# Performance work log

Measured on AMD Instinct MI355X. Metric: run time of the kernel, lower is better.

Reference implementation:

```python
import jax, jax.numpy as jnp
import numpy as np

N0, N1, N2 = 100000, 20000, 4000   # nodes per hierarchy level
F, H, C = 128, 128, 10             # num_features, hidden_dim, num_classes
E0, E1, E2 = 1600000, 320000, 64000  # intra-level edges (avg degree 16)
EPS = 1e-5                          # BatchNorm eps


def setup_inputs() -> dict:
    key = jax.random.key(0)
    ks = jax.random.split(key, 16)
    s = 0.05
    return {
        "x": jax.random.normal(ks[0], (N0, F), jnp.float32),
        "ei0": jax.random.randint(ks[1], (2, E0), 0, N0),
        "ei1": jax.random.randint(ks[2], (2, E1), 0, N1),
        "ei2": jax.random.randint(ks[3], (2, E2), 0, N2),
        "parent1": jax.random.randint(ks[4], (N0,), 0, N1),
        "parent2": jax.random.randint(ks[5], (N1,), 0, N2),
        "W0": jax.random.normal(ks[6], (F, H), jnp.float32) * s,
        "b0": jnp.zeros((H,), jnp.float32),
        "W1": jax.random.normal(ks[7], (H, H), jnp.float32) * s,
        "b1": jnp.zeros((H,), jnp.float32),
        "W2": jax.random.normal(ks[8], (H, H), jnp.float32) * s,
        "b2": jnp.zeros((H,), jnp.float32),
        "W3": jax.random.normal(ks[9], (2 * H, H), jnp.float32) * s,
        "b3": jnp.zeros((H,), jnp.float32),
        "W4": jax.random.normal(ks[10], (2 * H, C), jnp.float32) * s,
        "b4": jnp.zeros((C,), jnp.float32),
        "pW": jax.random.normal(ks[11], (4, H, H), jnp.float32) * s,
        "pb": jnp.zeros((4, H), jnp.float32),
        "pgamma": jnp.ones((4, H), jnp.float32),
        "pbeta": jnp.zeros((4, H), jnp.float32),
        "pmean": jax.random.normal(ks[12], (4, H), jnp.float32) * 0.1,
        "pvar": jax.random.uniform(ks[13], (4, H), jnp.float32, 0.5, 1.5),
    }


def _gcn(x, ei, W, b):
    # GCNConv: add self loops, symmetric D^-1/2 (A+I) D^-1/2 normalization.
    n = x.shape[0]
    loops = jnp.arange(n)
    row = jnp.concatenate([ei[0], loops])  # source nodes
    col = jnp.concatenate([ei[1], loops])  # target nodes
    deg = jax.ops.segment_sum(jnp.ones(row.shape, x.dtype), col, num_segments=n)
    dis = deg ** -0.5  # deg >= 1 because of self loops
    norm = dis[row] * dis[col]
    xw = x @ W
    out = jax.ops.segment_sum(norm[:, None] * xw[row], col, num_segments=n)
    return out + b


def _pool_nn(y, W, b, g, beta, mean, var):
    # SEPooling nn: Linear -> ReLU -> BatchNorm1d (eval mode, running stats)
    y = jax.nn.relu(y @ W + b)
    return (y - mean) * (g / jnp.sqrt(var + EPS)) + beta


def reference(x, ei0, ei1, ei2, parent1, parent2,
              W0, b0, W1, b1, W2, b2, W3, b3, W4, b4,
              pW, pb, pgamma, pbeta, pmean, pvar):
    relu = jax.nn.relu
    # down path (dropout is identity in eval mode)
    h0 = relu(_gcn(x, ei0, W0, b0))  # [N0,H]; stored skip xs[0]
    p = jax.ops.segment_sum(h0, parent1, num_segments=N1)  # scatter-add children -> parents
    x1 = relu(_pool_nn(p, pW[0], pb[0], pgamma[0], pbeta[0], pmean[0], pvar[0]))
    h1 = relu(_gcn(x1, ei1, W1, b1))  # [N1,H]; stored skip xs[1]
    p = jax.ops.segment_sum(h1, parent2, num_segments=N2)
    x2 = relu(_pool_nn(p, pW[1], pb[1], pgamma[1], pbeta[1], pmean[1], pvar[1]))
    # up path: conv, unpool (gather parent feature per child), concat skip
    h = relu(_gcn(x2, ei2, W2, b2))  # [N2,H]
    xu = relu(_pool_nn(h[parent2], pW[2], pb[2], pgamma[2], pbeta[2], pmean[2], pvar[2]))  # [N1,H]
    xc = jnp.concatenate([xu, h1], axis=1)  # [N1,2H]
    h = relu(_gcn(xc, ei1, W3, b3))  # [N1,H]
    xu = relu(_pool_nn(h[parent1], pW[3], pb[3], pgamma[3], pbeta[3], pmean[3], pvar[3]))  # [N0,H]
    xc = jnp.concatenate([xu, h0], axis=1)  # [N0,2H]
    out = _gcn(xc, ei0, W4, b4)  # [N0,C]
    return jax.nn.log_softmax(out, axis=-1)
```

## Files before the change

### kernel.cpp

```cpp
#include <hip/hip_runtime.h>
#include <math.h>

#define N0 100000
#define N1 20000
#define N2 4000
#define HDIM 128
#define E0C 1600000
#define E1C 320000
#define E2C 64000
#define EPSBN 1e-5f

typedef unsigned int u32;
typedef float f32x4 __attribute__((ext_vector_type(4)));
typedef short bf16x8 __attribute__((ext_vector_type(8)));

union FragU { uint4 u; bf16x8 h; };
__device__ __forceinline__ bf16x8 asbf(uint4 v) { FragU x; x.u = v; return x.h; }

__device__ __forceinline__ float bl(u32 p) { return __uint_as_float(p << 16); }
__device__ __forceinline__ float bh(u32 p) { return __uint_as_float(p & 0xFFFF0000u); }
__device__ __forceinline__ u32 pack2(float a, float b) {
    u32 ua = __float_as_uint(a), ub = __float_as_uint(b);
    ua = (ua + 0x7FFFu + ((ua >> 16) & 1u)) >> 16;
    ub = (ub + 0x7FFFu + ((ub >> 16) & 1u)) >> 16;
    return ua | (ub << 16);
}

#define OFF0 0
#define OFF1 (N0)
#define OFF2 (N0 + N1)
#define OFF3 (N0 + N1 + N2)
#define OFF4 (N0 + N1 + N2 + N1)
#define OFFT (N0 + N1 + N2 + N1 + N2)

#define S0 (E0C)
#define S1 (E0C + E1C)
#define S2 (E0C + E1C + E2C)
#define S3 (E0C + E1C + E2C + N0)
#define S4 (E0C + E1C + E2C + N0 + N1)

#define NBUCK ((OFFT + 1023) / 1024)
#define ITEMS_PER_BLK 2048
#define NBA ((S4 + ITEMS_PER_BLK - 1) / ITEMS_PER_BLK)
#define BH_N (NBUCK * NBA)
#define NBLK2 ((BH_N + 1023) / 1024)

#define NWMAT 9


__device__ __forceinline__ void item_full(int g,
    const int* __restrict__ ei0r, const int* __restrict__ ei0c,
    const int* __restrict__ ei1r, const int* __restrict__ ei1c,
    const int* __restrict__ ei2r, const int* __restrict__ ei2c,
    const int* __restrict__ p1, const int* __restrict__ p2,
    int& concat, int& payload)
{
    if (g < S0)      { concat = ei0c[g];             payload = ei0r[g]; }
    else if (g < S1) { int i = g - S0; concat = OFF1 + ei1c[i]; payload = ei1r[i]; }
    else if (g < S2) { int i = g - S1; concat = OFF2 + ei2c[i]; payload = ei2r[i]; }
    else if (g < S3) { int i = g - S2; concat = OFF3 + p1[i];   payload = i; }
    else             { int i = g - S3; concat = OFF4 + p2[i];   payload = i; }
}

__device__ __forceinline__ int item_concat(int g,
    const int* __restrict__ ei0c, const int* __restrict__ ei1c, const int* __restrict__ ei2c,
    const int* __restrict__ p1, const int* __restrict__ p2)
{
    if (g < S0)      return ei0c[g];
    else if (g < S1) return OFF1 + ei1c[g - S0];
    else if (g < S2) return OFF2 + ei2c[g - S1];
    else if (g < S3) return OFF3 + p1[g - S2];
    else             return OFF4 + p2[g - S3];
}

__global__ __launch_bounds__(256) void binhist_kernel(
    const int* __restrict__ ei0c, const int* __restrict__ ei1c, const int* __restrict__ ei2c,
    const int* __restrict__ p1, const int* __restrict__ p2,
    int* __restrict__ blockHist,
    const float* __restrict__ W0p, const float* __restrict__ W1p,
    const float* __restrict__ W2p, const float* __restrict__ W3p,
    const float* __restrict__ pWp, u32* __restrict__ Wpk)
{
    __shared__ int hist[NBUCK];
    int tid = threadIdx.x, blk = blockIdx.x;
    if (blk >= NBA) {
        int b = blk - NBA;
        const float* src;
        if (b == 0) src = W0p;
        else if (b == 1) src = W1p;
        else if (b == 2) src = W2p;
        else if (b == 3) src = W3p;
        else if (b == 4) src = W3p + 128 * 128;
        else src = pWp + (b - 5) * 128 * 128;
        u32* dst = Wpk + b * 8192;
        #pragma unroll
        for (int it = 0; it < 32; it++) {
            int flat = it * 256 + tid;
            int i = flat & 3;
            int ln = (flat >> 2) & 63;
            int s = (flat >> 8) & 3;
            int t = flat >> 10;
            int mm = ln & 15, qq = ln >> 4;
            int k0 = s * 32 + qq * 8 + 2 * i;
            int col = t * 16 + mm;
            dst[flat] = pack2(src[k0 * 128 + col], src[(k0 + 1) * 128 + col]);
        }
        return;
    }
    for (int i = tid; i < NBUCK; i += 256) hist[i] = 0;
    __syncthreads();
    int base = blk * ITEMS_PER_BLK;
    #pragma unroll
    for (int k = 0; k < ITEMS_PER_BLK / 256; k++) {
        int g = base + k * 256 + tid;
        if (g < S4) {
            int c = item_concat(g, ei0c, ei1c, ei2c, p1, p2);
            atomicAdd(&hist[c >> 10], 1);
        }
    }
    __syncthreads();
    for (int b = tid; b < NBUCK; b += 256) blockHist[b * NBA + blk] = hist[b];
}

__global__ __launch_bounds__(256) void scan_k1(const int* __restrict__ c, int* __restrict__ bsum, int n) {
    int t = threadIdx.x;
    int base = blockIdx.x * 1024 + t * 4;
    int s = 0;
    #pragma unroll
    for (int j = 0; j < 4; j++) {
        int idx = base + j;
        if (idx < n) s += c[idx];
    }
    #pragma unroll
    for (int o = 32; o > 0; o >>= 1) s += __shfl_down(s, o, 64);
    __shared__ int ws[4];
    if ((t & 63) == 0) ws[t >> 6] = s;
    __syncthreads();
    if (t == 0) bsum[blockIdx.x] = ws[0] + ws[1] + ws[2] + ws[3];
}

__global__ __launch_bounds__(256) void scan_k2(int* __restrict__ bsum, int* __restrict__ totalOut, int nb,
    const float* __restrict__ g, const float* __restrict__ beta,
    const float* __restrict__ mean, const float* __restrict__ var,
    float* __restrict__ scale, float* __restrict__ shift)
{
    int t = threadIdx.x;
    #pragma unroll
    for (int j = 0; j < 2; j++) {
        int i = j * 256 + t;
        float s = g[i] * rsqrtf(var[i] + EPSBN);
        scale[i] = s;
        shift[i] = beta[i] - mean[i] * s;
    }
    int v = (t < nb) ? bsum[t] : 0;
    __shared__ int ts[256];
    ts[t] = v;
    __syncthreads();
    for (int o = 1; o < 256; o <<= 1) {
        int u = (t >= o) ? ts[t - o] : 0;
        __syncthreads();
        ts[t] += u;
        __syncthreads();
    }
    if (t < nb) bsum[t] = ts[t] - v;
    if (t == nb - 1) *totalOut = ts[t];
}

__global__ __launch_bounds__(256) void scan_k3(const int* __restrict__ c, const int* __restrict__ bsum,
                                               const int* __restrict__ total,
                                               int* __restrict__ S, int n) {
    int t = threadIdx.x;
    int base = blockIdx.x * 1024 + t * 4;
    int v[4];
    #pragma unroll
    for (int j = 0; j < 4; j++) v[j] = (base + j < n) ? c[base + j] : 0;
    int tsum = v[0] + v[1] + v[2] + v[3];
    __shared__ int ts[256];
    ts[t] = tsum;
    __syncthreads();
    for (int o = 1; o < 256; o <<= 1) {
        int u = (t >= o) ? ts[t - o] : 0;
        __syncthreads();
        ts[t] += u;
        __syncthreads();
    }
    int run = bsum[blockIdx.x] + ts[t] - tsum;
    #pragma unroll
    for (int j = 0; j < 4; j++) {
        if (base + j < n) { S[base + j] = run; run += v[j]; }
    }
    if (blockIdx.x == 0 && t == 0) S[n] = *total;
}

__global__ __launch_bounds__(256) void binfill_kernel(
    const int* __restrict__ ei0r, const int* __restrict__ ei0c,
    const int* __restrict__ ei1r, const int* __restrict__ ei1c,
    const int* __restrict__ ei2r, const int* __restrict__ ei2c,
    const int* __restrict__ p1, const int* __restrict__ p2,
    const int* __restrict__ OfsAbs, u32* __restrict__ binPair)
{
    __shared__ int cur[NBUCK];
    int tid = threadIdx.x, blk = blockIdx.x;
    for (int i = tid; i < NBUCK; i += 256) cur[i] = OfsAbs[i * NBA + blk];
    __syncthreads();
    int base = blk * ITEMS_PER_BLK;
    #pragma unroll
    for (int k = 0; k < ITEMS_PER_BLK / 256; k++) {
        int g = base + k * 256 + tid;
        if (g < S4) {
            int c, p;
            item_full(g, ei0r, ei0c, ei1r, ei1c, ei2r, ei2c, p1, p2, c, p);
            int pos = atomicAdd(&cur[c >> 10], 1);
            binPair[pos] = ((u32)(c & 1023) << 17) | (u32)p;
        }
    }
}

__global__ __launch_bounds__(1024) void bucket_build_kernel(
    const u32* __restrict__ binPair, const int* __restrict__ OfsAbs,
    int* __restrict__ rpAll, int* __restrict__ srcU,
    float* __restrict__ dis0, float* __restrict__ dis1, float* __restrict__ dis2)
{
    __shared__ int cnt_l[1024];
    __shared__ int rp_l[1024];
    __shared__ int wsum[16];
    int b = blockIdx.x, tid = threadIdx.x;
    int start = OfsAbs[b * NBA];
    int end = (b + 1 < NBUCK) ? OfsAbs[(b + 1) * NBA] : S4;
    int d0 = b << 10;
    int nd = OFFT - d0; if (nd > 1024) nd = 1024;

    cnt_l[tid] = 0;
    __syncthreads();
    for (int i = start + tid; i < end; i += 1024) {
        u32 e = binPair[i];
        atomicAdd(&cnt_l[e >> 17], 1);
    }
    __syncthreads();
    int v = cnt_l[tid];
    int lane = tid & 63, wv = tid >> 6;
    int s = v;
    #pragma unroll
    for (int o = 1; o < 64; o <<= 1) {
        int u = __shfl_up(s, o, 64);
        if (lane >= o) s += u;
    }
    if (lane == 63) wsum[wv] = s;
    __syncthreads();
    if (wv == 0) {
        int t2 = (lane < 16) ? wsum[lane] : 0;
        #pragma unroll
        for (int o = 1; o < 16; o <<= 1) {
            int u = __shfl_up(t2, o, 64);
            if (lane >= o) t2 += u;
        }
        if (lane < 16) wsum[lane] = t2;
    }
    __syncthreads();
    int incl = s + (wv ? wsum[wv - 1] : 0);
    rp_l[tid] = incl - v;
    __syncthreads();
    if (tid < nd) {
        int g = d0 + tid;
        rpAll[g] = start + rp_l[tid];
        float dv = rsqrtf((float)(v + 1));
        if (g < OFF1) dis0[g] = dv;
        else if (g < OFF2) dis1[g - OFF1] = dv;
        else if (g < OFF3) dis2[g - OFF2] = dv;
    }
    if (b == NBUCK - 1 && tid == 0) rpAll[OFFT] = S4;
    __syncthreads();
    for (int i = start + tid; i < end; i += 1024) {
        u32 e = binPair[i];
        int pos = start + atomicAdd(&rp_l[e >> 17], 1);
        srcU[pos] = (int)(e & 0x1FFFFu);
    }
}


#define G128_LOAD(sym, off) u32 sym = y[(long long)srcl[e + off] * 64 + lane]

__global__ __launch_bounds__(256) void gather128_kernel(
    const int* __restrict__ rp, const int* __restrict__ srcl,
    const u32* __restrict__ y, const float* __restrict__ dis,
    const float* __restrict__ bias, u32* __restrict__ h, int n)
{
    int wid = (int)((blockIdx.x * 256 + threadIdx.x) >> 6);
    int lane = threadIdx.x & 63;
    if (wid >= n) return;
    u32 self = y[(long long)wid * 64 + lane];
    float ax = bl(self), ay = bh(self);
    int e = rp[wid], e1 = rp[wid + 1];
    for (; e + 7 < e1; e += 8) {
        G128_LOAD(p0, 0); G128_LOAD(p1, 1); G128_LOAD(p2, 2); G128_LOAD(p3, 3);
        G128_LOAD(p4, 4); G128_LOAD(p5, 5); G128_LOAD(p6, 6); G128_LOAD(p7, 7);
        ax += ((bl(p0) + bl(p1)) + (bl(p2) + bl(p3))) + ((bl(p4) + bl(p5)) + (bl(p6) + bl(p7)));
        ay += ((bh(p0) + bh(p1)) + (bh(p2) + bh(p3))) + ((bh(p4) + bh(p5)) + (bh(p6) + bh(p7)));
    }
    if (e + 3 < e1) {
        G128_LOAD(p0, 0); G128_LOAD(p1, 1); G128_LOAD(p2, 2); G128_LOAD(p3, 3);
        ax += (bl(p0) + bl(p1)) + (bl(p2) + bl(p3));
        ay += (bh(p0) + bh(p1)) + (bh(p2) + bh(p3));
        e += 4;
    }
    if (e + 1 < e1) {
        G128_LOAD(p0, 0); G128_LOAD(p1, 1);
        ax += bl(p0) + bl(p1);
        ay += bh(p0) + bh(p1);
        e += 2;
    }
    if (e < e1) {
        G128_LOAD(p0, 0);
        ax += bl(p0); ay += bh(p0);
    }
    float d = dis[wid];
    float2 b = ((const float2*)bias)[lane];
    float r0 = fmaxf(fmaf(d, ax, b.x), 0.f);
    float r1 = fmaxf(fmaf(d, ay, b.y), 0.f);
    h[(long long)wid * 64 + lane] = pack2(r0, r1);
}

__global__ __launch_bounds__(256) void gather10_lsm_kernel(
    const int* __restrict__ rp, const int* __restrict__ srcl,
    const u32* __restrict__ y4, const float* __restrict__ dis,
    const float* __restrict__ bias, float* __restrict__ out, int n)
{
    int c = blockIdx.x * blockDim.x + threadIdx.x;
    if (c >= n) return;
    float acc[10];
    {
        long long base = (long long)c * 8;
        uint4 q = *(const uint4*)(y4 + base);
        u32 q4 = y4[base + 4];
        acc[0] = bl(q.x); acc[1] = bh(q.x);
        acc[2] = bl(q.y); acc[3] = bh(q.y);
        acc[4] = bl(q.z); acc[5] = bh(q.z);
        acc[6] = bl(q.w); acc[7] = bh(q.w);
        acc[8] = bl(q4);  acc[9] = bh(q4);
    }
    int e = rp[c], e1 = rp[c + 1];
    for (; e + 3 < e1; e += 4) {
        long long bA = (long long)srcl[e] * 8;
        long long bB = (long long)srcl[e + 1] * 8;
        long long bC = (long long)srcl[e + 2] * 8;
        long long bD = (long long)srcl[e + 3] * 8;
        uint4 qa = *(const uint4*)(y4 + bA); u32 qa4 = y4[bA + 4];
        uint4 qb = *(const uint4*)(y4 + bB); u32 qb4 = y4[bB + 4];
        uint4 qc = *(const uint4*)(y4 + bC); u32 qc4 = y4[bC + 4];
        uint4 qd = *(const uint4*)(y4 + bD); u32 qd4 = y4[bD + 4];
        acc[0] += (bl(qa.x) + bl(qb.x)) + (bl(qc.x) + bl(qd.x));
        acc[1] += (bh(qa.x) + bh(qb.x)) + (bh(qc.x) + bh(qd.x));
        acc[2] += (bl(qa.y) + bl(qb.y)) + (bl(qc.y) + bl(qd.y));
        acc[3] += (bh(qa.y) + bh(qb.y)) + (bh(qc.y) + bh(qd.y));
        acc[4] += (bl(qa.z) + bl(qb.z)) + (bl(qc.z) + bl(qd.z));
        acc[5] += (bh(qa.z) + bh(qb.z)) + (bh(qc.z) + bh(qd.z));
        acc[6] += (bl(qa.w) + bl(qb.w)) + (bl(qc.w) + bl(qd.w));
        acc[7] += (bh(qa.w) + bh(qb.w)) + (bh(qc.w) + bh(qd.w));
        acc[8] += (bl(qa4) + bl(qb4)) + (bl(qc4) + bl(qd4));
        acc[9] += (bh(qa4) + bh(qb4)) + (bh(qc4) + bh(qd4));
    }
    for (; e < e1; e++) {
        long long bA = (long long)srcl[e] * 8;
        uint4 qa = *(const uint4*)(y4 + bA);
        u32 qa4 = y4[bA + 4];
        acc[0] += bl(qa.x); acc[1] += bh(qa.x);
        acc[2] += bl(qa.y); acc[3] += bh(qa.y);
        acc[4] += bl(qa.z); acc[5] += bh(qa.z);
        acc[6] += bl(qa.w); acc[7] += bh(qa.w);
        acc[8] += bl(qa4);  acc[9] += bh(qa4);
    }
    float d = dis[c];
    float m = -1e30f;
    #pragma unroll
    for (int k = 0; k < 10; k++) {
        acc[k] = fmaf(d, acc[k], bias[k]);
        m = fmaxf(m, acc[k]);
    }
    float s = 0.f;
    #pragma unroll
    for (int k = 0; k < 10; k++) s += expf(acc[k] - m);
    float ls = logf(s);
    #pragma unroll
    for (int k = 0; k < 10; k++) out[(long long)c * 10 + k] = acc[k] - m - ls;
}

__global__ __launch_bounds__(256) void mm128_kernel(
    const void* __restrict__ Av, const u32* __restrict__ Wp,
    u32* __restrict__ out, int M,
    const float* __restrict__ dis,
    const u32* __restrict__ gsrc, const int* __restrict__ gidx,
    const float* __restrict__ bias,
    const float* __restrict__ bnscale, const float* __restrict__ bnshift,
    int pool, int afp32,
    const int* __restrict__ pp, const int* __restrict__ childl, int apool)
{
    __shared__ u32 WL[8192];
    int tid = threadIdx.x;
    {
        const uint4* ws4 = (const uint4*)Wp;
        uint4* wd4 = (uint4*)WL;
        #pragma unroll
        for (int it = 0; it < 8; it++) wd4[it * 256 + tid] = ws4[it * 256 + tid];
    }
    __syncthreads();

    int lane = tid & 63;
    int w = tid >> 6;
    int m = lane & 15, q = lane >> 4;
    int row = blockIdx.x * 64 + w * 16 + m;
    bool live = (row < M);

    uint4 xb[4];
    if (live) {
        if (apool) {
            float fa[32];
            #pragma unroll
            for (int i = 0; i < 32; i++) fa[i] = 0.f;
            const u32* Hb = (const u32*)Av;
            int e = pp[row], eE = pp[row + 1];
            for (; e < eE; e++) {
                long long cb = (long long)childl[e] * 64;
                #pragma unroll
                for (int s = 0; s < 4; s++) {
                    uint4 vv = *(const uint4*)(Hb + cb + s * 16 + q * 4);
                    fa[s * 8 + 0] += bl(vv.x); fa[s * 8 + 1] += bh(vv.x);
                    fa[s * 8 + 2] += bl(vv.y); fa[s * 8 + 3] += bh(vv.y);
                    fa[s * 8 + 4] += bl(vv.z); fa[s * 8 + 5] += bh(vv.z);
                    fa[s * 8 + 6] += bl(vv.w); fa[s * 8 + 7] += bh(vv.w);
                }
            }
            #pragma unroll
            for (int s = 0; s < 4; s++) {
                xb[s].x = pack2(fa[s * 8 + 0], fa[s * 8 + 1]);
                xb[s].y = pack2(fa[s * 8 + 2], fa[s * 8 + 3]);
                xb[s].z = pack2(fa[s * 8 + 4], fa[s * 8 + 5]);
                xb[s].w = pack2(fa[s * 8 + 6], fa[s * 8 + 7]);
            }
        } else if (afp32) {
            const float* Af = (const float*)Av;
            #pragma unroll
            for (int s = 0; s < 4; s++) {
                const float4* p = (const float4*)(Af + (long long)row * 128 + s * 32 + q * 8);
                float4 f0 = p[0], f1 = p[1];
                xb[s].x = pack2(f0.x, f0.y);
                xb[s].y = pack2(f0.z, f0.w);
                xb[s].z = pack2(f1.x, f1.y);
                xb[s].w = pack2(f1.z, f1.w);
            }
        } else {
            const u32* Ab = (const u32*)Av;
            #pragma unroll
            for (int s = 0; s < 4; s++)
                xb[s] = *(const uint4*)(Ab + (long long)row * 64 + s * 16 + q * 4);
        }
    } else {
        xb[0] = xb[1] = xb[2] = xb[3] = make_uint4(0u, 0u, 0u, 0u);
    }

    float d = 1.0f;
    if (dis && live) d = dis[row];
    long long gbase = (gsrc && live) ? (long long)gidx[row] * 64 : 0;

    #pragma unroll
    for (int t = 0; t < 8; t++) {
        f32x4 acc = {0.f, 0.f, 0.f, 0.f};
        #pragma unroll
        for (int s = 0; s < 4; s++) {
            uint4 wa = *(const uint4*)&WL[((t * 4 + s) * 64 + lane) * 4];
            acc = __builtin_amdgcn_mfma_f32_16x16x32_bf16(asbf(wa), asbf(xb[s]), acc, 0, 0, 0);
        }
        if (live) {
            float v0 = acc[0], v1 = acc[1], v2 = acc[2], v3 = acc[3];
            int cbase = t * 16 + q * 4;
            if (gsrc) {
                uint2 g = *(const uint2*)(gsrc + gbase + (cbase >> 1));
                v0 += bl(g.x); v1 += bh(g.x);
                v2 += bl(g.y); v3 += bh(g.y);
            }
            if (pool) {
                float4 bb = *(const float4*)(bias + cbase);
                float4 sc = *(const float4*)(bnscale + cbase);
                float4 sh = *(const float4*)(bnshift + cbase);
                v0 = fmaxf(fmaxf(v0 + bb.x, 0.f) * sc.x + sh.x, 0.f);
                v1 = fmaxf(fmaxf(v1 + bb.y, 0.f) * sc.y + sh.y, 0.f);
                v2 = fmaxf(fmaxf(v2 + bb.z, 0.f) * sc.z + sh.z, 0.f);
                v3 = fmaxf(fmaxf(v3 + bb.w, 0.f) * sc.w + sh.w, 0.f);
            }
            v0 *= d; v1 *= d; v2 *= d; v3 *= d;
            uint2 st;
            st.x = pack2(v0, v1);
            st.y = pack2(v2, v3);
            *(uint2*)(out + (long long)row * 64 + (cbase >> 1)) = st;
        }
    }
}

#define TLP 68
__global__ __launch_bounds__(256) void mm128x2_kernel(
    const u32* __restrict__ Av, const u32* __restrict__ Wa, const u32* __restrict__ Wb,
    u32* __restrict__ out, int M,
    const float* __restrict__ dis2,
    const float* __restrict__ bias1,
    const float* __restrict__ bnscale1, const float* __restrict__ bnshift1,
    const int* __restrict__ pp, const int* __restrict__ childl, int apool)
{
    __shared__ u32 WL[8192];
    __shared__ u32 TL[64 * TLP];
    int tid = threadIdx.x;
    {
        const uint4* ws4 = (const uint4*)Wa;
        uint4* wd4 = (uint4*)WL;
        #pragma unroll
        for (int it = 0; it < 8; it++) wd4[it * 256 + tid] = ws4[it * 256 + tid];
    }
    __syncthreads();

    int lane = tid & 63;
    int w = tid >> 6;
    int m = lane & 15, q = lane >> 4;
    int row = blockIdx.x * 64 + w * 16 + m;
    bool live = (row < M);

    uint4 xb[4];
    if (live) {
        if (apool) {
            float fa[32];
            #pragma unroll
            for (int i = 0; i < 32; i++) fa[i] = 0.f;
            int e = pp[row], eE = pp[row + 1];
            for (; e < eE; e++) {
                long long cb = (long long)childl[e] * 64;
                #pragma unroll
                for (int s = 0; s < 4; s++) {
                    uint4 vv = *(const uint4*)(Av + cb + s * 16 + q * 4);
                    fa[s * 8 + 0] += bl(vv.x); fa[s * 8 + 1] += bh(vv.x);
                    fa[s * 8 + 2] += bl(vv.y); fa[s * 8 + 3] += bh(vv.y);
                    fa[s * 8 + 4] += bl(vv.z); fa[s * 8 + 5] += bh(vv.z);
                    fa[s * 8 + 6] += bl(vv.w); fa[s * 8 + 7] += bh(vv.w);
                }
            }
            #pragma unroll
            for (int s = 0; s < 4; s++) {
                xb[s].x = pack2(fa[s * 8 + 0], fa[s * 8 + 1]);
                xb[s].y = pack2(fa[s * 8 + 2], fa[s * 8 + 3]);
                xb[s].z = pack2(fa[s * 8 + 4], fa[s * 8 + 5]);
                xb[s].w = pack2(fa[s * 8 + 6], fa[s * 8 + 7]);
            }
        } else {
            #pragma unroll
            for (int s = 0; s < 4; s++)
                xb[s] = *(const uint4*)(Av + (long long)row * 64 + s * 16 + q * 4);
        }
    } else {
        xb[0] = xb[1] = xb[2] = xb[3] = make_uint4(0u, 0u, 0u, 0u);
    }

    u32* tl = TL + (w * 16 + m) * TLP;

    #pragma unroll
    for (int t = 0; t < 8; t++) {
        f32x4 acc = {0.f, 0.f, 0.f, 0.f};
        #pragma unroll
        for (int s = 0; s < 4; s++) {
            uint4 wa4 = *(const uint4*)&WL[((t * 4 + s) * 64 + lane) * 4];
            acc = __builtin_amdgcn_mfma_f32_16x16x32_bf16(asbf(wa4), asbf(xb[s]), acc, 0, 0, 0);
        }
        int cbase = t * 16 + q * 4;
        float4 bb = *(const float4*)(bias1 + cbase);
        float4 sc = *(const float4*)(bnscale1 + cbase);
        float4 sh = *(const float4*)(bnshift1 + cbase);
        float v0 = fmaxf(fmaxf(acc[0] + bb.x, 0.f) * sc.x + sh.x, 0.f);
        float v1 = fmaxf(fmaxf(acc[1] + bb.y, 0.f) * sc.y + sh.y, 0.f);
        float v2 = fmaxf(fmaxf(acc[2] + bb.z, 0.f) * sc.z + sh.z, 0.f);
        float v3 = fmaxf(fmaxf(acc[3] + bb.w, 0.f) * sc.w + sh.w, 0.f);
        uint2 st;
        st.x = pack2(v0, v1);
        st.y = pack2(v2, v3);
        *(uint2*)&tl[t * 8 + q * 2] = st;
    }
    __syncthreads();
    {
        const uint4* ws4 = (const uint4*)Wb;
        uint4* wd4 = (uint4*)WL;
        #pragma unroll
        for (int it = 0; it < 8; it++) wd4[it * 256 + tid] = ws4[it * 256 + tid];
    }
    __syncthreads();

    #pragma unroll
    for (int s = 0; s < 4; s++)
        xb[s] = *(const uint4*)&tl[s * 16 + q * 4];
    float d = 1.0f;
    if (dis2 && live) d = dis2[row];

    #pragma unroll
    for (int t = 0; t < 8; t++) {
        f32x4 acc = {0.f, 0.f, 0.f, 0.f};
        #pragma unroll
        for (int s = 0; s < 4; s++) {
            uint4 wa4 = *(const uint4*)&WL[((t * 4 + s) * 64 + lane) * 4];
            acc = __builtin_amdgcn_mfma_f32_16x16x32_bf16(asbf(wa4), asbf(xb[s]), acc, 0, 0, 0);
        }
        if (live) {
            int cbase = t * 16 + q * 4;
            float v0 = acc[0] * d, v1 = acc[1] * d, v2 = acc[2] * d, v3 = acc[3] * d;
            uint2 st;
            st.x = pack2(v0, v1);
            st.y = pack2(v2, v3);
            *(uint2*)(out + (long long)row * 64 + (cbase >> 1)) = st;
        }
    }
}

__global__ __launch_bounds__(256) void mm128_mm10_kernel(
    const u32* __restrict__ Av, const u32* __restrict__ Wp,
    const float* __restrict__ W10,
    float* __restrict__ out10, int M,
    const float* __restrict__ bias1,
    const float* __restrict__ bnscale1, const float* __restrict__ bnshift1)
{
    __shared__ u32 WL[8192];
    __shared__ u32 TL[64 * TLP];
    __shared__ float Ws[128 * 10];
    int tid = threadIdx.x;
    {
        const uint4* ws4 = (const uint4*)Wp;
        uint4* wd4 = (uint4*)WL;
        #pragma unroll
        for (int it = 0; it < 8; it++) wd4[it * 256 + tid] = ws4[it * 256 + tid];
    }
    for (int i = tid; i < 1280; i += 256) Ws[i] = W10[i];
    __syncthreads();

    int lane = tid & 63;
    int w = tid >> 6;
    int m = lane & 15, q = lane >> 4;
    int row = blockIdx.x * 64 + w * 16 + m;
    bool live = (row < M);

    uint4 xb[4];
    if (live) {
        #pragma unroll
        for (int s = 0; s < 4; s++)
            xb[s] = *(const uint4*)(Av + (long long)row * 64 + s * 16 + q * 4);
    } else {
        xb[0] = xb[1] = xb[2] = xb[3] = make_uint4(0u, 0u, 0u, 0u);
    }

    u32* tl = TL + (w * 16 + m) * TLP;

    #pragma unroll
    for (int t = 0; t < 8; t++) {
        f32x4 acc = {0.f, 0.f, 0.f, 0.f};
        #pragma unroll
        for (int s = 0; s < 4; s++) {
            uint4 wa4 = *(const uint4*)&WL[((t * 4 + s) * 64 + lane) * 4];
            acc = __builtin_amdgcn_mfma_f32_16x16x32_bf16(asbf(wa4), asbf(xb[s]), acc, 0, 0, 0);
        }
        int cbase = t * 16 + q * 4;
        float4 bb = *(const float4*)(bias1 + cbase);
        float4 sc = *(const float4*)(bnscale1 + cbase);
        float4 sh = *(const float4*)(bnshift1 + cbase);
        float v0 = fmaxf(fmaxf(acc[0] + bb.x, 0.f) * sc.x + sh.x, 0.f);
        float v1 = fmaxf(fmaxf(acc[1] + bb.y, 0.f) * sc.y + sh.y, 0.f);
        float v2 = fmaxf(fmaxf(acc[2] + bb.z, 0.f) * sc.z + sh.z, 0.f);
        float v3 = fmaxf(fmaxf(acc[3] + bb.w, 0.f) * sc.w + sh.w, 0.f);
        uint2 st;
        st.x = pack2(v0, v1);
        st.y = pack2(v2, v3);
        *(uint2*)&tl[t * 8 + q * 2] = st;
    }
    __syncthreads();

    int base = blockIdx.x * 64;
    for (int slot = tid; slot < 640; slot += 256) {
        int r = slot / 10, cc = slot % 10;
        if (base + r < M) {
            const u32* tr = &TL[r * TLP];
            float acc = 0.f;
            #pragma unroll
            for (int k2 = 0; k2 < 64; k2++) {
                u32 p = tr[k2];
                acc += bl(p) * Ws[(2 * k2) * 10 + cc];
                acc += bh(p) * Ws[(2 * k2 + 1) * 10 + cc];
            }
            out10[(long long)(base + r) * 10 + cc] = acc;
        }
    }
}

__global__ __launch_bounds__(256) void mm10p_kernel(
    const u32* __restrict__ A, const float* __restrict__ W,
    u32* __restrict__ outp, int M,
    const float* __restrict__ dis,
    const float* __restrict__ gsrc, const int* __restrict__ gidx)
{
    __shared__ float Ws[128 * 10];
    for (int i = threadIdx.x; i < 1280; i += 256) Ws[i] = W[i];
    __syncthreads();
    int row = blockIdx.x * blockDim.x + threadIdx.x;
    if (row >= M) return;
    const uint4* a = (const uint4*)(A + (long long)row * 64);
    float acc[10] = {0, 0, 0, 0, 0, 0, 0, 0, 0, 0};
    #pragma unroll 4
    for (int i = 0; i < 16; i++) {
        uint4 av = a[i];
        int k = i * 8;
        float f[8] = { bl(av.x), bh(av.x), bl(av.y), bh(av.y),
                       bl(av.z), bh(av.z), bl(av.w), bh(av.w) };
        #pragma unroll
        for (int j = 0; j < 8; j++) {
            #pragma unroll
            for (int cc = 0; cc < 10; cc++)
                acc[cc] += f[j] * Ws[(k + j) * 10 + cc];
        }
    }
    float d = dis[row];
    const float* g = gsrc + (long long)gidx[row] * 10;
    long long base = (long long)row * 8;
    #pragma unroll
    for (int j = 0; j < 5; j++) {
        float v0 = (acc[2 * j] + g[2 * j]) * d;
        float v1 = (acc[2 * j + 1] + g[2 * j + 1]) * d;
        outp[base + j] = pack2(v0, v1);
    }
}


extern "C" void kernel_launch(void* const* d_in, const int* in_sizes, int n_in,
                              void* d_out, int out_size, void* d_ws, size_t ws_size,
                              hipStream_t stream) {
    const float* x       = (const float*)d_in[0];
    const int*   ei0     = (const int*)d_in[1];
    const int*   ei1     = (const int*)d_in[2];
    const int*   ei2     = (const int*)d_in[3];
    const int*   parent1 = (const int*)d_in[4];
    const int*   parent2 = (const int*)d_in[5];
    const float* W0 = (const float*)d_in[6];
    const float* b0 = (const float*)d_in[7];
    const float* W1 = (const float*)d_in[8];
    const float* b1 = (const float*)d_in[9];
    const float* W2 = (const float*)d_in[10];
    const float* b2 = (const float*)d_in[11];
    const float* W3 = (const float*)d_in[12];
    const float* b3 = (const float*)d_in[13];
    const float* W4 = (const float*)d_in[14];
    const float* b4 = (const float*)d_in[15];
    const float* pW = (const float*)d_in[16];
    const float* pb = (const float*)d_in[17];
    const float* pg = (const float*)d_in[18];
    const float* pbeta = (const float*)d_in[19];
    const float* pmean = (const float*)d_in[20];
    const float* pvar  = (const float*)d_in[21];
    float* out = (float*)d_out;

    char* ws = (char*)d_ws;
    size_t off = 0;
    auto alloc = [&](size_t nbytes) -> char* {
        char* p = ws + off;
        off += ((nbytes + 255) / 256) * 256;
        return p;
    };
    float* dis0 = (float*)alloc(N0 * 4);
    float* dis1 = (float*)alloc(N1 * 4);
    float* dis2 = (float*)alloc(N2 * 4);
    float* bnscale = (float*)alloc(4 * HDIM * 4);
    float* bnshift = (float*)alloc(4 * HDIM * 4);
    float* W1b = (float*)alloc((size_t)N1 * 10 * 4);
    u32* Y   = (u32*)alloc((size_t)N0 * 64 * 4);
    u32* H0  = (u32*)alloc((size_t)N0 * 64 * 4);
    u32* H1  = (u32*)alloc((size_t)N1 * 64 * 4);
    u32* HU1 = (u32*)alloc((size_t)N1 * 64 * 4);
    u32* H2  = (u32*)alloc((size_t)N2 * 64 * 4);
    u32* V2  = (u32*)alloc((size_t)N2 * 64 * 4);
    u32* Y4p = (u32*)alloc((size_t)N0 * 8 * 4);
    u32* Wpk = (u32*)alloc((size_t)NWMAT * 8192 * 4);
    int* rpAll = (int*)alloc((size_t)(OFFT + 1) * 4);
    int* srcU  = (int*)alloc((size_t)S4 * 4);
    int* blockHist = (int*)alloc((size_t)BH_N * 4);
    int* OfsAbs    = (int*)alloc((size_t)(BH_N + 1) * 4);
    u32* binPair   = (u32*)alloc((size_t)S4 * 4);
    int* bsum   = (int*)alloc(NBLK2 * 4);
    int* totalb = (int*)alloc(4);

    const int B = 256;
    auto G = [](long long t) { return (unsigned)((t + 255) / 256); };
    auto G64 = [](long long m) { return (unsigned)((m + 63) / 64); };

    binhist_kernel<<<NBA + NWMAT, B, 0, stream>>>(
        ei0 + E0C, ei1 + E1C, ei2 + E2C, parent1, parent2, blockHist,
        W0, W1, W2, W3, pW, Wpk);
    scan_k1<<<NBLK2, B, 0, stream>>>(blockHist, bsum, BH_N);
    scan_k2<<<1, B, 0, stream>>>(bsum, totalb, NBLK2, pg, pbeta, pmean, pvar, bnscale, bnshift);
    scan_k3<<<NBLK2, B, 0, stream>>>(blockHist, bsum, totalb, OfsAbs, BH_N);
    binfill_kernel<<<NBA, B, 0, stream>>>(
        ei0, ei0 + E0C, ei1, ei1 + E1C, ei2, ei2 + E2C, parent1, parent2, OfsAbs, binPair);
    bucket_build_kernel<<<NBUCK, 1024, 0, stream>>>(
        binPair, OfsAbs, rpAll, srcU, dis0, dis1, dis2);

    mm128_kernel<<<G64(N0), B, 0, stream>>>(
        x, Wpk + 0 * 8192, Y, N0, dis0, nullptr, nullptr, nullptr, nullptr, nullptr, 0, 1,
        nullptr, nullptr, 0);
    gather128_kernel<<<G((long long)N0 * 64), B, 0, stream>>>(rpAll + OFF0, srcU, Y, dis0, b0, H0, N0);

    mm128x2_kernel<<<G64(N1), B, 0, stream>>>(
        H0, Wpk + 5 * 8192, Wpk + 1 * 8192, Y, N1, dis1,
        pb, bnscale, bnshift, rpAll + OFF3, srcU, 1);
    gather128_kernel<<<G((long long)N1 * 64), B, 0, stream>>>(rpAll + OFF1, srcU, Y, dis1, b1, H1, N1);

    mm128x2_kernel<<<G64(N2), B, 0, stream>>>(
        H1, Wpk + 6 * 8192, Wpk + 2 * 8192, Y, N2, dis2,
        pb + 128, bnscale + 128, bnshift + 128, rpAll + OFF4, srcU, 1);
    gather128_kernel<<<G((long long)N2 * 64), B, 0, stream>>>(rpAll + OFF2, srcU, Y, dis2, b2, H2, N2);

    mm128x2_kernel<<<G64(N2), B, 0, stream>>>(
        H2, Wpk + 7 * 8192, Wpk + 3 * 8192, V2, N2, nullptr,
        pb + 256, bnscale + 256, bnshift + 256, nullptr, nullptr, 0);

    mm128_kernel<<<G64(N1), B, 0, stream>>>(
        H1, Wpk + 4 * 8192, Y, N1, dis1, V2, parent2, nullptr, nullptr, nullptr, 0, 0,
        nullptr, nullptr, 0);
    gather128_kernel<<<G((long long)N1 * 64), B, 0, stream>>>(rpAll + OFF1, srcU, Y, dis1, b3, HU1, N1);

    mm128_mm10_kernel<<<G64(N1), B, 0, stream>>>(
        HU1, Wpk + 8 * 8192, W4, W1b, N1, pb + 384, bnscale + 384, bnshift + 384);

    mm10p_kernel<<<G(N0), B, 0, stream>>>(H0, W4 + 128 * 10, Y4p, N0, dis0, W1b, parent1);
    gather10_lsm_kernel<<<G(N0), B, 0, stream>>>(rpAll + OFF0, srcU, Y4p, dis0, b4, out, N0);
}
```

Before: 385.6 us.

## Slice level-0 GCN gather per XCD and fold x@W0 and H0@W4 into earlier kernels

The x@W0 product now runs inside the binhist launch and writes Y in a column-sliced layout, eight slices of 16 features each. A new gather kernel processes one slice at a time, starting with a slice chosen from the hardware XCC id, and pulls row chunks from atomic counters. The aim is to keep each slice resident in that XCD's L2 cache during the random-access neighbour gather. The H0@W4 skip projection is moved into extra blocks of the first mm128x2 launch and stored as a T0 buffer, so the final mm10p kernel only adds and scales. In exchange, dis is now applied per edge instead of being prescaled into Y, and the design relies on the XCD-to-slice affinity actually holding.

Measured after the change: 777.4 us. +101.6%, slower.

```diff
diff --git a/kernel.cpp b/kernel.cpp
--- a/kernel.cpp
+++ b/kernel.cpp
@@ -46,6 +46,11 @@
 #define NBLK2 ((BH_N + 1023) / 1024)
 
 #define NWMAT 9
+#define G64N0 ((N0 + 63) / 64)
+
+#define SLICES 8
+#define CHROWS 128
+#define CHN ((N0 + CHROWS - 1) / CHROWS)
 
 
 __device__ __forceinline__ void item_full(int g,
@@ -79,11 +84,29 @@
     int* __restrict__ blockHist,
     const float* __restrict__ W0p, const float* __restrict__ W1p,
     const float* __restrict__ W2p, const float* __restrict__ W3p,
-    const float* __restrict__ pWp, u32* __restrict__ Wpk)
+    const float* __restrict__ pWp, u32* __restrict__ Wpk,
+    const float* __restrict__ xin, u32* __restrict__ Yout)
 {
     __shared__ int hist[NBUCK];
+    __shared__ u32 WL[8192];
     int tid = threadIdx.x, blk = blockIdx.x;
-    if (blk >= NBA) {
+    if (blk < NBA) {
+        for (int i = tid; i < NBUCK; i += 256) hist[i] = 0;
+        __syncthreads();
+        int base = blk * ITEMS_PER_BLK;
+        #pragma unroll
+        for (int k = 0; k < ITEMS_PER_BLK / 256; k++) {
+            int g = base + k * 256 + tid;
+            if (g < S4) {
+                int c = item_concat(g, ei0c, ei1c, ei2c, p1, p2);
+                atomicAdd(&hist[c >> 10], 1);
+            }
+        }
+        __syncthreads();
+        for (int b = tid; b < NBUCK; b += 256) blockHist[b * NBA + blk] = hist[b];
+        return;
+    }
+    if (blk < NBA + NWMAT) {
         int b = blk - NBA;
         const float* src;
         if (b == 0) src = W0p;
@@ -107,19 +130,54 @@
         }
         return;
     }
-    for (int i = tid; i < NBUCK; i += 256) hist[i] = 0;
-    __syncthreads();
-    int base = blk * ITEMS_PER_BLK;
-    #pragma unroll
-    for (int k = 0; k < ITEMS_PER_BLK / 256; k++) {
-        int g = base + k * 256 + tid;
-        if (g < S4) {
-            int c = item_concat(g, ei0c, ei1c, ei2c, p1, p2);
-            atomicAdd(&hist[c >> 10], 1);
-        }
-    }
-    __syncthreads();
-    for (int b = tid; b < NBUCK; b += 256) blockHist[b * NBA + blk] = hist[b];
+    int bb = blk - (NBA + NWMAT);
+    #pragma unroll
+    for (int it = 0; it < 32; it++) {
+        int flat = it * 256 + tid;
+        int i = flat & 3;
+        int ln = (flat >> 2) & 63;
+        int s = (flat >> 8) & 3;
+        int t = flat >> 10;
+        int mm = ln & 15, qq = ln >> 4;
+        int k0 = s * 32 + qq * 8 + 2 * i;
+        int col = t * 16 + mm;
+        WL[flat] = pack2(W0p[k0 * 128 + col], W0p[(k0 + 1) * 128 + col]);
+    }
+    __syncthreads();
+    int lane = tid & 63;
+    int w = tid >> 6;
+    int m = lane & 15, q = lane >> 4;
+    int row = bb * 64 + w * 16 + m;
+    bool live = (row < N0);
+    uint4 xb[4];
+    if (live) {
+        #pragma unroll
+        for (int s = 0; s < 4; s++) {
+            const float4* p = (const float4*)(xin + (long long)row * 128 + s * 32 + q * 8);
+            float4 f0 = p[0], f1 = p[1];
+            xb[s].x = pack2(f0.x, f0.y);
+            xb[s].y = pack2(f0.z, f0.w);
+            xb[s].z = pack2(f1.x, f1.y);
+            xb[s].w = pack2(f1.z, f1.w);
+        }
+    } else {
+        xb[0] = xb[1] = xb[2] = xb[3] = make_uint4(0u, 0u, 0u, 0u);
+    }
+    #pragma unroll
+    for (int t = 0; t < 8; t++) {
+        f32x4 acc = {0.f, 0.f, 0.f, 0.f};
+        #pragma unroll
+        for (int s = 0; s < 4; s++) {
+            uint4 wa = *(const uint4*)&WL[((t * 4 + s) * 64 + lane) * 4];
+            acc = __builtin_amdgcn_mfma_f32_16x16x32_bf16(asbf(wa), asbf(xb[s]), acc, 0, 0, 0);
+        }
+        if (live) {
+            uint2 st;
+            st.x = pack2(acc[0], acc[1]);
+            st.y = pack2(acc[2], acc[3]);
+            *(uint2*)(Yout + ((long long)t * N0 + row) * 8 + q * 2) = st;
+        }
+    }
 }
 
 __global__ __launch_bounds__(256) void scan_k1(const int* __restrict__ c, int* __restrict__ bsum, int n) {
@@ -277,6 +335,65 @@
     }
 }
 
+
+__global__ __launch_bounds__(256) void gather128sx_kernel(
+    const int* __restrict__ rp, const int* __restrict__ srcl,
+    const u32* __restrict__ ys, const float* __restrict__ dis,
+    const float* __restrict__ bias, u32* __restrict__ h, int* __restrict__ ctr)
+{
+    __shared__ int curC;
+    int tid = threadIdx.x;
+    int wv = tid >> 6, lane = tid & 63;
+    int eg = lane >> 3, l8 = lane & 7;
+    int xcc = __builtin_amdgcn_s_getreg(20 | (3 << 11)) & 7;
+    for (int k = 0; k < SLICES; k++) {
+        int xq = (xcc + k) & 7;
+        const u32* Y = ys + (long long)xq * (N0 * 8);
+        const float2* bslice = (const float2*)bias + xq * 8;
+        while (true) {
+            __syncthreads();
+            if (tid == 0) curC = atomicAdd(&ctr[xq], 1);
+            __syncthreads();
+            int c = curC;
+            if (c >= CHN) break;
+            int rbase = c * CHROWS + wv * (CHROWS / 4);
+            for (int rr = 0; rr < CHROWS / 4; rr++) {
+                int r = rbase + rr;
+                if (r >= N0) break;
+                int e0 = rp[r], e1 = rp[r + 1];
+                float ax = 0.f, ay = 0.f;
+                {
+                    u32 sv = Y[(long long)r * 8 + l8];
+                    float ds = (eg == 0) ? dis[r] : 0.f;
+                    ax = ds * bl(sv); ay = ds * bh(sv);
+                }
+                for (int e = e0; e < e1; e += 16) {
+                    int eiA = e + eg;
+                    int eiB = eiA + 8;
+                    bool vA = eiA < e1, vB = eiB < e1;
+                    int sA = vA ? __builtin_nontemporal_load(srcl + eiA) : r;
+                    int sB = vB ? __builtin_nontemporal_load(srcl + eiB) : r;
+                    u32 pA = Y[(long long)sA * 8 + l8];
+                    u32 pB = Y[(long long)sB * 8 + l8];
+                    float dsA = vA ? dis[sA] : 0.f;
+                    float dsB = vB ? dis[sB] : 0.f;
+                    ax = fmaf(dsA, bl(pA), ax); ay = fmaf(dsA, bh(pA), ay);
+                    ax = fmaf(dsB, bl(pB), ax); ay = fmaf(dsB, bh(pB), ay);
+                }
+                ax += __shfl_xor(ax, 8, 64);  ay += __shfl_xor(ay, 8, 64);
+                ax += __shfl_xor(ax, 16, 64); ay += __shfl_xor(ay, 16, 64);
+                ax += __shfl_xor(ax, 32, 64); ay += __shfl_xor(ay, 32, 64);
+                if (eg == 0) {
+                    float d = dis[r];
+                    float2 b = bslice[l8];
+                    u32 o = pack2(fmaxf(fmaf(d, ax, b.x), 0.f),
+                                  fmaxf(fmaf(d, ay, b.y), 0.f));
+                    __builtin_nontemporal_store(o, h + (long long)r * 64 + xq * 8 + l8);
+                }
+            }
+        }
+    }
+}
 
 #define G128_LOAD(sym, off) u32 sym = y[(long long)srcl[e + off] * 64 + lane]
 
@@ -502,11 +619,36 @@
     const float* __restrict__ dis2,
     const float* __restrict__ bias1,
     const float* __restrict__ bnscale1, const float* __restrict__ bnshift1,
-    const int* __restrict__ pp, const int* __restrict__ childl, int apool)
+    const int* __restrict__ pp, const int* __restrict__ childl, int apool,
+    const float* __restrict__ W10, float* __restrict__ T0out, int Mt0)
 {
     __shared__ u32 WL[8192];
     __shared__ u32 TL[64 * TLP];
     int tid = threadIdx.x;
+    int nmm = (M + 63) >> 6;
+    if ((int)blockIdx.x >= nmm) {
+        int rowt = ((int)blockIdx.x - nmm) * 256 + tid;
+        if (rowt < Mt0) {
+            const uint4* a = (const uint4*)(Av + (long long)rowt * 64);
+            float acc[10] = {0, 0, 0, 0, 0, 0, 0, 0, 0, 0};
+            #pragma unroll 4
+            for (int i = 0; i < 16; i++) {
+                uint4 av = a[i];
+                int k = i * 8;
+                float f[8] = { bl(av.x), bh(av.x), bl(av.y), bh(av.y),
+                               bl(av.z), bh(av.z), bl(av.w), bh(av.w) };
+                #pragma unroll
+                for (int j = 0; j < 8; j++) {
+                    #pragma unroll
+                    for (int cc = 0; cc < 10; cc++)
+                        acc[cc] += f[j] * W10[(k + j) * 10 + cc];
+                }
+            }
+            #pragma unroll
+            for (int cc = 0; cc < 10; cc++) T0out[(long long)rowt * 10 + cc] = acc[cc];
+        }
+        return;
+    }
     {
         const uint4* ws4 = (const uint4*)Wa;
         uint4* wd4 = (uint4*)WL;
@@ -689,39 +831,21 @@
     }
 }
 
-__global__ __launch_bounds__(256) void mm10p_kernel(
-    const u32* __restrict__ A, const float* __restrict__ W,
-    u32* __restrict__ outp, int M,
-    const float* __restrict__ dis,
-    const float* __restrict__ gsrc, const int* __restrict__ gidx)
-{
-    __shared__ float Ws[128 * 10];
-    for (int i = threadIdx.x; i < 1280; i += 256) Ws[i] = W[i];
-    __syncthreads();
-    int row = blockIdx.x * blockDim.x + threadIdx.x;
+__global__ __launch_bounds__(256) void mm10p2_kernel(
+    const float* __restrict__ T0, const float* __restrict__ gsrc,
+    const int* __restrict__ gidx, const float* __restrict__ dis,
+    u32* __restrict__ outp, int M)
+{
+    int row = blockIdx.x * 256 + threadIdx.x;
     if (row >= M) return;
-    const uint4* a = (const uint4*)(A + (long long)row * 64);
-    float acc[10] = {0, 0, 0, 0, 0, 0, 0, 0, 0, 0};
-    #pragma unroll 4
-    for (int i = 0; i < 16; i++) {
-        uint4 av = a[i];
-        int k = i * 8;
-        float f[8] = { bl(av.x), bh(av.x), bl(av.y), bh(av.y),
-                       bl(av.z), bh(av.z), bl(av.w), bh(av.w) };
-        #pragma unroll
-        for (int j = 0; j < 8; j++) {
-            #pragma unroll
-            for (int cc = 0; cc < 10; cc++)
-                acc[cc] += f[j] * Ws[(k + j) * 10 + cc];
-        }
-    }
     float d = dis[row];
+    const float* t = T0 + (long long)row * 10;
     const float* g = gsrc + (long long)gidx[row] * 10;
     long long base = (long long)row * 8;
     #pragma unroll
     for (int j = 0; j < 5; j++) {
-        float v0 = (acc[2 * j] + g[2 * j]) * d;
-        float v1 = (acc[2 * j + 1] + g[2 * j + 1]) * d;
+        float v0 = (t[2 * j] + g[2 * j]) * d;
+        float v1 = (t[2 * j + 1] + g[2 * j + 1]) * d;
         outp[base + j] = pack2(v0, v1);
     }
 }
@@ -767,6 +891,7 @@
     float* bnscale = (float*)alloc(4 * HDIM * 4);
     float* bnshift = (float*)alloc(4 * HDIM * 4);
     float* W1b = (float*)alloc((size_t)N1 * 10 * 4);
+    float* T0  = (float*)alloc((size_t)N0 * 10 * 4);
     u32* Y   = (u32*)alloc((size_t)N0 * 64 * 4);
     u32* H0  = (u32*)alloc((size_t)N0 * 64 * 4);
     u32* H1  = (u32*)alloc((size_t)N1 * 64 * 4);
@@ -782,14 +907,16 @@
     u32* binPair   = (u32*)alloc((size_t)S4 * 4);
     int* bsum   = (int*)alloc(NBLK2 * 4);
     int* totalb = (int*)alloc(4);
+    int* ctr    = (int*)alloc(SLICES * 4);
 
     const int B = 256;
     auto G = [](long long t) { return (unsigned)((t + 255) / 256); };
     auto G64 = [](long long m) { return (unsigned)((m + 63) / 64); };
 
-    binhist_kernel<<<NBA + NWMAT, B, 0, stream>>>(
+    binhist_kernel<<<NBA + NWMAT + G64N0, B, 0, stream>>>(
         ei0 + E0C, ei1 + E1C, ei2 + E2C, parent1, parent2, blockHist,
-        W0, W1, W2, W3, pW, Wpk);
+        W0, W1, W2, W3, pW, Wpk, x, Y);
+    hipMemsetAsync(ctr, 0, SLICES * 4, stream);
     scan_k1<<<NBLK2, B, 0, stream>>>(blockHist, bsum, BH_N);
     scan_k2<<<1, B, 0, stream>>>(bsum, totalb, NBLK2, pg, pbeta, pmean, pvar, bnscale, bnshift);
     scan_k3<<<NBLK2, B, 0, stream>>>(blockHist, bsum, totalb, OfsAbs, BH_N);
@@ -798,24 +925,25 @@
     bucket_build_kernel<<<NBUCK, 1024, 0, stream>>>(
         binPair, OfsAbs, rpAll, srcU, dis0, dis1, dis2);
 
-    mm128_kernel<<<G64(N0), B, 0, stream>>>(
-        x, Wpk + 0 * 8192, Y, N0, dis0, nullptr, nullptr, nullptr, nullptr, nullptr, 0, 1,
-        nullptr, nullptr, 0);
-    gather128_kernel<<<G((long long)N0 * 64), B, 0, stream>>>(rpAll + OFF0, srcU, Y, dis0, b0, H0, N0);
-
-    mm128x2_kernel<<<G64(N1), B, 0, stream>>>(
+    gather128sx_kernel<<<2048, B, 0, stream>>>(
+        rpAll + OFF0, srcU, Y, dis0, b0, H0, ctr);
+
+    mm128x2_kernel<<<G64(N1) + G(N0), B, 0, stream>>>(
         H0, Wpk + 5 * 8192, Wpk + 1 * 8192, Y, N1, dis1,
-        pb, bnscale, bnshift, rpAll + OFF3, srcU, 1);
+        pb, bnscale, bnshift, rpAll + OFF3, srcU, 1,
+        W4 + 128 * 10, T0, N0);
     gather128_kernel<<<G((long long)N1 * 64), B, 0, stream>>>(rpAll + OFF1, srcU, Y, dis1, b1, H1, N1);
 
     mm128x2_kernel<<<G64(N2), B, 0, stream>>>(
         H1, Wpk + 6 * 8192, Wpk + 2 * 8192, Y, N2, dis2,
-        pb + 128, bnscale + 128, bnshift + 128, rpAll + OFF4, srcU, 1);
+        pb + 128, bnscale + 128, bnshift + 128, rpAll + OFF4, srcU, 1,
+        nullptr, nullptr, 0);
     gather128_kernel<<<G((long long)N2 * 64), B, 0, stream>>>(rpAll + OFF2, srcU, Y, dis2, b2, H2, N2);
 
     mm128x2_kernel<<<G64(N2), B, 0, stream>>>(
         H2, Wpk + 7 * 8192, Wpk + 3 * 8192, V2, N2, nullptr,
-        pb + 256, bnscale + 256, bnshift + 256, nullptr, nullptr, 0);
+        pb + 256, bnscale + 256, bnshift + 256, nullptr, nullptr, 0,
+        nullptr, nullptr, 0);
 
     mm128_kernel<<<G64(N1), B, 0, stream>>>(
         H1, Wpk + 4 * 8192, Y, N1, dis1, V2, parent2, nullptr, nullptr, nullptr, 0, 0,
@@ -825,6 +953,6 @@
     mm128_mm10_kernel<<<G64(N1), B, 0, stream>>>(
         HU1, Wpk + 8 * 8192, W4, W1b, N1, pb + 384, bnscale + 384, bnshift + 384);
 
-    mm10p_kernel<<<G(N0), B, 0, stream>>>(H0, W4 + 128 * 10, Y4p, N0, dis0, W1b, parent1);
+    mm10p2_kernel<<<G(N0), B, 0, stream>>>(T0, W1b, parent1, dis0, Y4p, N0);
     gather10_lsm_kernel<<<G(N0), B, 0, stream>>>(rpAll + OFF0, srcU, Y4p, dis0, b4, out, N0);
 }
```

## Hoist H0·W4 skip projection into earlier pool kernel as extra blocks

Applied to the files above, without the earlier changes.

The projection of the H0 skip features onto the lower half of W4 (N0×128 → 10) is moved out of the final mm10p kernel. It now runs as extra blocks appended to the first mm128x2 launch, which is small (N1 rows) and would otherwise underfill the GPU. The final kernel then only adds the gathered parent term, scales by dis and packs. This hides the H0 read and GEMV work behind an under-occupied kernel, at the cost of an extra fp32 T0 buffer write and read. The extra blocks also read W10 directly from global memory instead of staging it in LDS.

Result: faster. 377.1 us, median of 3 (-2.2%).

```diff
diff --git a/kernel.cpp b/kernel.cpp
--- a/kernel.cpp
+++ b/kernel.cpp
@@ -502,11 +502,36 @@
     const float* __restrict__ dis2,
     const float* __restrict__ bias1,
     const float* __restrict__ bnscale1, const float* __restrict__ bnshift1,
-    const int* __restrict__ pp, const int* __restrict__ childl, int apool)
+    const int* __restrict__ pp, const int* __restrict__ childl, int apool,
+    const float* __restrict__ W10, float* __restrict__ T0out, int Mt0)
 {
     __shared__ u32 WL[8192];
     __shared__ u32 TL[64 * TLP];
     int tid = threadIdx.x;
+    int nmm = (M + 63) >> 6;
+    if ((int)blockIdx.x >= nmm) {
+        int rowt = ((int)blockIdx.x - nmm) * 256 + tid;
+        if (rowt < Mt0) {
+            const uint4* a = (const uint4*)(Av + (long long)rowt * 64);
+            float acc[10] = {0, 0, 0, 0, 0, 0, 0, 0, 0, 0};
+            #pragma unroll 4
+            for (int i = 0; i < 16; i++) {
+                uint4 av = a[i];
+                int k = i * 8;
+                float f[8] = { bl(av.x), bh(av.x), bl(av.y), bh(av.y),
+                               bl(av.z), bh(av.z), bl(av.w), bh(av.w) };
+                #pragma unroll
+                for (int j = 0; j < 8; j++) {
+                    #pragma unroll
+                    for (int cc = 0; cc < 10; cc++)
+                        acc[cc] += f[j] * W10[(k + j) * 10 + cc];
+                }
+            }
+            #pragma unroll
+            for (int cc = 0; cc < 10; cc++) T0out[(long long)rowt * 10 + cc] = acc[cc];
+        }
+        return;
+    }
     {
         const uint4* ws4 = (const uint4*)Wa;
         uint4* wd4 = (uint4*)WL;
@@ -689,39 +714,21 @@
     }
 }
 
-__global__ __launch_bounds__(256) void mm10p_kernel(
-    const u32* __restrict__ A, const float* __restrict__ W,
-    u32* __restrict__ outp, int M,
-    const float* __restrict__ dis,
-    const float* __restrict__ gsrc, const int* __restrict__ gidx)
-{
-    __shared__ float Ws[128 * 10];
-    for (int i = threadIdx.x; i < 1280; i += 256) Ws[i] = W[i];
-    __syncthreads();
-    int row = blockIdx.x * blockDim.x + threadIdx.x;
+__global__ __launch_bounds__(256) void mm10p2_kernel(
+    const float* __restrict__ T0, const float* __restrict__ gsrc,
+    const int* __restrict__ gidx, const float* __restrict__ dis,
+    u32* __restrict__ outp, int M)
+{
+    int row = blockIdx.x * 256 + threadIdx.x;
     if (row >= M) return;
-    const uint4* a = (const uint4*)(A + (long long)row * 64);
-    float acc[10] = {0, 0, 0, 0, 0, 0, 0, 0, 0, 0};
-    #pragma unroll 4
-    for (int i = 0; i < 16; i++) {
-        uint4 av = a[i];
-        int k = i * 8;
-        float f[8] = { bl(av.x), bh(av.x), bl(av.y), bh(av.y),
-                       bl(av.z), bh(av.z), bl(av.w), bh(av.w) };
-        #pragma unroll
-        for (int j = 0; j < 8; j++) {
-            #pragma unroll
-            for (int cc = 0; cc < 10; cc++)
-                acc[cc] += f[j] * Ws[(k + j) * 10 + cc];
-        }
-    }
     float d = dis[row];
+    const float* t = T0 + (long long)row * 10;
     const float* g = gsrc + (long long)gidx[row] * 10;
     long long base = (long long)row * 8;
     #pragma unroll
     for (int j = 0; j < 5; j++) {
-        float v0 = (acc[2 * j] + g[2 * j]) * d;
-        float v1 = (acc[2 * j + 1] + g[2 * j + 1]) * d;
+        float v0 = (t[2 * j] + g[2 * j]) * d;
+        float v1 = (t[2 * j + 1] + g[2 * j + 1]) * d;
         outp[base + j] = pack2(v0, v1);
     }
 }
@@ -767,6 +774,7 @@
     float* bnscale = (float*)alloc(4 * HDIM * 4);
     float* bnshift = (float*)alloc(4 * HDIM * 4);
     float* W1b = (float*)alloc((size_t)N1 * 10 * 4);
+    float* T0  = (float*)alloc((size_t)N0 * 10 * 4);
     u32* Y   = (u32*)alloc((size_t)N0 * 64 * 4);
     u32* H0  = (u32*)alloc((size_t)N0 * 64 * 4);
     u32* H1  = (u32*)alloc((size_t)N1 * 64 * 4);
@@ -803,19 +811,22 @@
         nullptr, nullptr, 0);
     gather128_kernel<<<G((long long)N0 * 64), B, 0, stream>>>(rpAll + OFF0, srcU, Y, dis0, b0, H0, N0);
 
-    mm128x2_kernel<<<G64(N1), B, 0, stream>>>(
+    mm128x2_kernel<<<G64(N1) + G(N0), B, 0, stream>>>(
         H0, Wpk + 5 * 8192, Wpk + 1 * 8192, Y, N1, dis1,
-        pb, bnscale, bnshift, rpAll + OFF3, srcU, 1);
+        pb, bnscale, bnshift, rpAll + OFF3, srcU, 1,
+        W4 + 128 * 10, T0, N0);
     gather128_kernel<<<G((long long)N1 * 64), B, 0, stream>>>(rpAll + OFF1, srcU, Y, dis1, b1, H1, N1);
 
     mm128x2_kernel<<<G64(N2), B, 0, stream>>>(
         H1, Wpk + 6 * 8192, Wpk + 2 * 8192, Y, N2, dis2,
-        pb + 128, bnscale + 128, bnshift + 128, rpAll + OFF4, srcU, 1);
+        pb + 128, bnscale + 128, bnshift + 128, rpAll + OFF4, srcU, 1,
+        nullptr, nullptr, 0);
     gather128_kernel<<<G((long long)N2 * 64), B, 0, stream>>>(rpAll + OFF2, srcU, Y, dis2, b2, H2, N2);
 
     mm128x2_kernel<<<G64(N2), B, 0, stream>>>(
         H2, Wpk + 7 * 8192, Wpk + 3 * 8192, V2, N2, nullptr,
-        pb + 256, bnscale + 256, bnshift + 256, nullptr, nullptr, 0);
+        pb + 256, bnscale + 256, bnshift + 256, nullptr, nullptr, 0,
+        nullptr, nullptr, 0);
 
     mm128_kernel<<<G64(N1), B, 0, stream>>>(
         H1, Wpk + 4 * 8192, Y, N1, dis1, V2, parent2, nullptr, nullptr, nullptr, 0, 0,
@@ -825,6 +836,6 @@
     mm128_mm10_kernel<<<G64(N1), B, 0, stream>>>(
         HU1, Wpk + 8 * 8192, W4, W1b, N1, pb + 384, bnscale + 384, bnshift + 384);
 
-    mm10p_kernel<<<G(N0), B, 0, stream>>>(H0, W4 + 128 * 10, Y4p, N0, dis0, W1b, parent1);
+    mm10p2_kernel<<<G(N0), B, 0, stream>>>(T0, W1b, parent1, dis0, Y4p, N0);
     gather10_lsm_kernel<<<G(N0), B, 0, stream>>>(rpAll + OFF0, srcU, Y4p, dis0, b4, out, N0);
 }
```
